# Kernel tuning notes

Measured on AMD Instinct MI355X. Metric: run time of the kernel, lower is better.

Reference implementation:

```python
import jax, jax.numpy as jnp
import numpy as np
from jax import lax

N, P = 64, 7
C1, H1 = 256, 56
C2, H2 = 512, 28
C3, H3 = 1024, 14
HID1, HID2, HID3 = 256, 768, 1792
MLP1, MLP2, OUT = 3584, 1792, 512


def setup_inputs() -> dict:
    key = jax.random.key(0)
    ks = jax.random.split(key, 32)
    x1 = jax.random.normal(ks[0], (N, C1, H1, H1), jnp.float32)
    x2 = jax.random.normal(ks[1], (N, C2, H2, H2), jnp.float32)
    x3 = jax.random.normal(ks[2], (N, C3, H3, H3), jnp.float32)
    a = jax.random.randint(ks[3], (N, P, 2), 0, 56)
    b = jax.random.randint(ks[4], (N, P, 2), 0, 56)
    lo, hi = jnp.minimum(a, b), jnp.maximum(a, b)
    patchs = jnp.stack([lo[..., 0], hi[..., 0], lo[..., 1], hi[..., 1]], axis=-1)
    drop = jax.random.bernoulli(ks[5], 0.1, (N, P))
    patchs = jnp.where(drop[..., None], 0, patchs).astype(jnp.int32)

    def lin(k, o, i):
        return jax.random.normal(k, (o, i), jnp.float32) * 0.02

    def vec(k, o):
        return jax.random.normal(k, (o,), jnp.float32) * 0.02

    inp = {
        'x1': x1, 'x2': x2, 'x3': x3, 'patchs': patchs,
        # LSTM weights, torch gate order (i,f,g,o); bias = b_ih + b_hh combined
        'l1_wih': lin(ks[6], 4 * HID1, 256),  'l1_whh': lin(ks[7], 4 * HID1, HID1),  'l1_b': vec(ks[8], 4 * HID1),
        'l2_wih': lin(ks[9], 4 * HID2, 768),  'l2_whh': lin(ks[10], 4 * HID2, HID2), 'l2_b': vec(ks[11], 4 * HID2),
        'l3_wih': lin(ks[12], 4 * HID3, 1792),'l3_whh': lin(ks[13], 4 * HID3, HID3), 'l3_b': vec(ks[14], 4 * HID3),
        'aw1': lin(ks[15], MLP1, P * HID3), 'ab1': vec(ks[16], MLP1),
        'aw2': lin(ks[17], MLP2, MLP1),     'ab2': vec(ks[18], MLP2),
        'aw3': lin(ks[19], P, MLP2),        'ab3': vec(ks[20], P),
        'fw':  lin(ks[21], OUT, HID3),      'fb':  vec(ks[22], OUT),
    }
    return inp


def _crop_avg(x, patchs, num, den):
    """Batched data-dependent crop + avg-pool via 2D integral image.
    x: [N,C,H,W]; patchs: [N,P,4] ints (y0,y1,x0,x1) at 56-scale. Returns [N,P,C]."""
    y0 = (patchs[..., 0] * num) // den
    y1 = (patchs[..., 1] * num) // den
    x0 = (patchs[..., 2] * num) // den
    x1 = (patchs[..., 3] * num) // den
    S = jnp.cumsum(jnp.cumsum(x, axis=2), axis=3)
    S = jnp.pad(S, ((0, 0), (0, 0), (1, 0), (1, 0)))  # [N,C,H+1,W+1]
    bidx = jnp.arange(x.shape[0])[:, None]

    def g(Y, X):
        return S[bidx, :, Y, X]  # advanced idx split by ':' -> [N,P,C]

    tot = g(y1 + 1, x1 + 1) - g(y0, x1 + 1) - g(y1 + 1, x0) + g(y0, x0)
    area = ((y1 - y0 + 1) * (x1 - x0 + 1)).astype(x.dtype)[..., None]
    avg = tot / area
    zero = jnp.all(patchs == 0, axis=-1)  # all-zero box -> zero feature
    return jnp.where(zero[..., None], jnp.zeros((), x.dtype), avg)


def _lstm(x, wih, whh, b):
    """Single-layer batch-first LSTM, torch gate order i,f,g,o. x: [N,T,D] -> [N,T,H]."""
    Nb, T, _ = x.shape
    H = whh.shape[1]
    xg = jnp.einsum('ntd,gd->ntg', x, wih) + b  # precompute input gates

    def step(carry, xt):
        h, c = carry
        gates = xt + h @ whh.T
        i, f, g, o = jnp.split(gates, 4, axis=-1)
        c = jax.nn.sigmoid(f) * c + jax.nn.sigmoid(i) * jnp.tanh(g)
        h = jax.nn.sigmoid(o) * jnp.tanh(c)
        return (h, c), h

    h0 = jnp.zeros((Nb, H), x.dtype)
    _, hs = lax.scan(step, (h0, h0), jnp.swapaxes(xg, 0, 1))
    return jnp.swapaxes(hs, 0, 1)


def reference(x1, x2, x3, patchs,
              l1_wih, l1_whh, l1_b, l2_wih, l2_whh, l2_b, l3_wih, l3_whh, l3_b,
              aw1, ab1, aw2, ab2, aw3, ab3, fw, fb):
    local1 = _crop_avg(x1, patchs, 55, 55)                     # [N,7,256]
    rnn1 = _lstm(local1, l1_wih, l1_whh, l1_b)                 # [N,7,256]
    local2 = jnp.concatenate([_crop_avg(x2, patchs, 27, 55), rnn1], axis=2)   # [N,7,768]
    rnn2 = _lstm(local2, l2_wih, l2_whh, l2_b)                 # [N,7,768]
    local3 = jnp.concatenate([_crop_avg(x3, patchs, 13, 55), rnn2], axis=2)   # [N,7,1792]
    rnn3 = _lstm(local3, l3_wih, l3_whh, l3_b)                 # [N,7,1792]
    # attention pooling (dropout = identity in eval)
    flat = rnn3.reshape(rnn3.shape[0], -1)                     # [N,7*1792]
    h = jax.nn.relu(flat @ aw1.T + ab1)
    h = jax.nn.relu(h @ aw2.T + ab2)
    attn = jax.nn.relu(h @ aw3.T + ab3)                        # [N,7]
    alpha = jax.nn.softmax(attn, axis=1)
    feat = jnp.sum(rnn3 * alpha[:, :, None], axis=1)           # [N,1792]
    return feat @ fw.T + fb                                    # [N,512]
```

## Files before the change

### kernel.cpp

```cpp
#include <hip/hip_runtime.h>
#include <hip/hip_bf16.h>
#include <math.h>

#define NB 64
#define PP 7

typedef __attribute__((ext_vector_type(8))) short short8;
typedef __attribute__((ext_vector_type(4))) float f32x4;

static __device__ inline unsigned bf16r(float f) {
    unsigned u = __builtin_bit_cast(unsigned, f);
    u += 0x7fffu + ((u >> 16) & 1u);
    return u >> 16;
}
static __device__ inline unsigned pack2(float a, float b) {
    return bf16r(a) | (bf16r(b) << 16);
}

template<int H, int VEC, int GRP>
__device__ inline void crop_dev(
    int bx, int n, const float* __restrict__ x, const int* __restrict__ patchs,
    float* __restrict__ out, int C, int num, int den, int ldo, int col0)
{
    constexpr int USED = H / VEC;
    constexpr int PPWAVE = 64 / GRP;
    int tid = threadIdx.x, lane = tid & 63, wv = tid >> 6;
    int sub = lane / GRP, xl = lane & (GRP - 1);
    bool act = xl < USED;
    int c = bx * (4 * PPWAVE) + wv * PPWAVE + sub;

    int y0s[PP], yds[PP], x0s[PP], x1s[PP], zer[PP];
    float rarea[PP];
    #pragma unroll
    for (int p = 0; p < PP; ++p) {
        int p0 = patchs[(n * PP + p) * 4 + 0];
        int p1 = patchs[(n * PP + p) * 4 + 1];
        int p2 = patchs[(n * PP + p) * 4 + 2];
        int p3 = patchs[(n * PP + p) * 4 + 3];
        int y0 = p0 * num / den, y1 = p1 * num / den;
        int xx0 = p2 * num / den, xx1 = p3 * num / den;
        y0s[p] = y0; yds[p] = y1 - y0;
        x0s[p] = xx0; x1s[p] = xx1;
        rarea[p] = 1.f / (float)((y1 - y0 + 1) * (xx1 - xx0 + 1));
        zer[p] = (p0 | p1 | p2 | p3) == 0;
    }

    const float* pl = x + ((size_t)n * C + c) * (H * H) + (act ? xl * VEC : 0);

    float acc[PP][VEC];
    #pragma unroll
    for (int p = 0; p < PP; ++p)
        #pragma unroll
        for (int e = 0; e < VEC; ++e) acc[p][e] = 0.f;

    #pragma unroll 4
    for (int y = 0; y < H; ++y) {
        float v[VEC];
        if constexpr (VEC == 4) {
            float4 t = *reinterpret_cast<const float4*>(pl + y * H);
            v[0] = t.x; v[1] = t.y; v[2] = t.z; v[3] = t.w;
        } else {
            float2 t = *reinterpret_cast<const float2*>(pl + y * H);
            v[0] = t.x; v[1] = t.y;
        }
        #pragma unroll
        for (int p = 0; p < PP; ++p) {
            float m = ((unsigned)(y - y0s[p]) <= (unsigned)yds[p]) ? 1.f : 0.f;
            #pragma unroll
            for (int e = 0; e < VEC; ++e)
                acc[p][e] = fmaf(m, v[e], acc[p][e]);
        }
    }

    #pragma unroll
    for (int p = 0; p < PP; ++p) {
        float d = 0.f;
        #pragma unroll
        for (int e = 0; e < VEC; ++e) {
            int col = xl * VEC + e;
            if (col >= x0s[p] && col <= x1s[p]) d += acc[p][e];
        }
        #pragma unroll
        for (int off = GRP / 2; off >= 1; off >>= 1)
            d += __shfl_xor(d, off, 64);
        if (act && xl == 0)
            out[(size_t)(n * PP + p) * ldo + col0 + c] = zer[p] ? 0.f : d * rarea[p];
    }
}

__device__ inline void cvt_dev(
    int b, const float* __restrict__ in, uint4* __restrict__ out, int n8)
{
    int idx = b * 256 + threadIdx.x;
    if (idx >= n8) return;
    const float4* p = reinterpret_cast<const float4*>(in) + 2 * (size_t)idx;
    float4 a = p[0], bb = p[1];
    uint4 v;
    v.x = pack2(a.x, a.y); v.y = pack2(a.z, a.w);
    v.z = pack2(bb.x, bb.y); v.w = pack2(bb.z, bb.w);
    out[idx] = v;
}

__global__ __launch_bounds__(256) void prep_kernel(
    const float* __restrict__ x1, const float* __restrict__ x2,
    const float* __restrict__ x3, const int* __restrict__ patchs,
    float* __restrict__ local1, float* __restrict__ local2,
    float* __restrict__ local3,
    const float* __restrict__ l1_whh, uint4* __restrict__ whh1b,
    const float* __restrict__ l2_whh, uint4* __restrict__ whh2b,
    const float* __restrict__ l3_whh, uint4* __restrict__ whh3b)
{
    int b = blockIdx.x;
    if (b < 1024) {
        crop_dev<56, 4, 16>(b & 15, b >> 4, x1, patchs, local1, 256, 55, 55, 256, 0);
    } else if (b < 2048) {
        int bb = b - 1024;
        crop_dev<28, 4, 8>(bb & 15, bb >> 4, x2, patchs, local2, 512, 27, 55, 768, 0);
    } else if (b < 4096) {
        int bb = b - 2048;
        crop_dev<14, 2, 8>(bb & 31, bb >> 5, x3, patchs, local3, 1024, 13, 55, 1792, 0);
    } else if (b < 4224) {
        cvt_dev(b - 4096, l1_whh, whh1b, 32768);
    } else if (b < 5376) {
        cvt_dev(b - 4224, l2_whh, whh2b, 294912);
    } else {
        cvt_dev(b - 5376, l3_whh, whh3b, 1605632);
    }
}

template<int BN, bool WBF>
__global__ __launch_bounds__(256) void gemm_kernel(
    const float* __restrict__ X, int ldx,
    const void* __restrict__ Wp, int K,
    const float* __restrict__ bias,
    float* __restrict__ out, int ldo,
    int kchunk, int partial)
{
    constexpr int NF = BN / 64;
    __shared__ short Xs[64][72];
    __shared__ short Ws[BN][72];
    int tid = threadIdx.x;
    int lane = tid & 63, wv = tid >> 6;
    int m0 = blockIdx.y * 64;
    int o0 = blockIdx.x * BN;
    int z = blockIdx.z;
    int kbeg = z * kchunk, kend = kbeg + kchunk;

    f32x4 acc[4][NF];
    #pragma unroll
    for (int i = 0; i < 4; ++i)
        #pragma unroll
        for (int j = 0; j < NF; ++j)
            acc[i][j] = (f32x4){0.f, 0.f, 0.f, 0.f};

    for (int kb = kbeg; kb < kend; kb += 64) {
        #pragma unroll
        for (int i = 0; i < 2; ++i) {
            int cch = tid + 256 * i;
            int r = cch >> 3, col = (cch & 7) * 8;
            const float* src = X + (size_t)(m0 + r) * ldx + kb + col;
            float4 a = *reinterpret_cast<const float4*>(src);
            float4 b = *reinterpret_cast<const float4*>(src + 4);
            uint4 v;
            v.x = pack2(a.x, a.y); v.y = pack2(a.z, a.w);
            v.z = pack2(b.x, b.y); v.w = pack2(b.z, b.w);
            *reinterpret_cast<uint4*>(&Xs[r][col]) = v;
        }
        #pragma unroll
        for (int i = 0; i < 2 * NF; ++i) {
            int cch = tid + 256 * i;
            int r = cch >> 3, col = (cch & 7) * 8;
            if constexpr (WBF) {
                const short* srcw = (const short*)Wp + (size_t)(o0 + r) * K + kb + col;
                *reinterpret_cast<uint4*>(&Ws[r][col]) =
                    *reinterpret_cast<const uint4*>(srcw);
            } else {
                const float* srcw = (const float*)Wp + (size_t)(o0 + r) * K + kb + col;
                float4 c = *reinterpret_cast<const float4*>(srcw);
                float4 d = *reinterpret_cast<const float4*>(srcw + 4);
                uint4 w;
                w.x = pack2(c.x, c.y); w.y = pack2(c.z, c.w);
                w.z = pack2(d.x, d.y); w.w = pack2(d.z, d.w);
                *reinterpret_cast<uint4*>(&Ws[r][col]) = w;
            }
        }
        __syncthreads();
        #pragma unroll
        for (int kk = 0; kk < 64; kk += 32) {
            int ro = lane & 15, kof = kk + (lane >> 4) * 8;
            short8 b[NF];
            #pragma unroll
            for (int j = 0; j < NF; ++j)
                b[j] = *reinterpret_cast<const short8*>(
                    &Ws[wv * (BN / 4) + 16 * j + ro][kof]);
            #pragma unroll
            for (int i = 0; i < 4; ++i) {
                short8 a = *reinterpret_cast<const short8*>(&Xs[16 * i + ro][kof]);
                #pragma unroll
                for (int j = 0; j < NF; ++j)
                    acc[i][j] = __builtin_amdgcn_mfma_f32_16x16x32_bf16(
                        a, b[j], acc[i][j], 0, 0, 0);
            }
        }
        __syncthreads();
    }

    float* dst = out;
    if (partial) dst += (size_t)z * (gridDim.y * 64) * ldo;
    int mr = (lane >> 4) * 4;
    #pragma unroll
    for (int j = 0; j < NF; ++j) {
        int o = o0 + wv * (BN / 4) + 16 * j + (lane & 15);
        float bv = (!partial && bias) ? bias[o] : 0.f;
        #pragma unroll
        for (int i = 0; i < 4; ++i) {
            #pragma unroll
            for (int r = 0; r < 4; ++r) {
                int m = m0 + 16 * i + mr + r;
                dst[(size_t)m * ldo + o] = acc[i][j][r] + bv;
            }
        }
    }
}

__global__ __launch_bounds__(256) void reduce_kernel(
    const float* __restrict__ partial, int S, int M, int O,
    const float* __restrict__ bias, int relu, float* __restrict__ out)
{
    int idx = blockIdx.x * 256 + threadIdx.x;
    int tot = M * O;
    if (idx >= tot) return;
    float v = bias[idx % O];
    for (int s = 0; s < S; ++s) v += partial[(size_t)s * tot + idx];
    if (relu) v = fmaxf(v, 0.f);
    out[idx] = v;
}

__global__ __launch_bounds__(256) void lstm_cell_kernel(
    const float* __restrict__ partial, int S,
    const float* __restrict__ xgt, int ldxg,
    float* __restrict__ h, float* __restrict__ c,
    float* __restrict__ dest, int Hd, int ldd, int first)
{
    int idx = blockIdx.x * 256 + threadIdx.x;
    int q = Hd >> 2;
    if (idx >= NB * q) return;
    int n = idx / q, j4 = (idx - n * q) * 4;
    int H4 = 4 * Hd;

    f32x4 g[4];
    #pragma unroll
    for (int gi = 0; gi < 4; ++gi)
        g[gi] = *reinterpret_cast<const f32x4*>(xgt + (size_t)n * ldxg + gi * Hd + j4);
    if (!first) {
        for (int s = 0; s < S; ++s) {
            const float* pr = partial + ((size_t)s * NB + n) * H4;
            #pragma unroll
            for (int gi = 0; gi < 4; ++gi)
                g[gi] += *reinterpret_cast<const f32x4*>(pr + gi * Hd + j4);
        }
    }
    f32x4 cp = (f32x4){0.f, 0.f, 0.f, 0.f};
    if (!first) cp = *reinterpret_cast<const f32x4*>(c + (size_t)n * Hd + j4);

    f32x4 cn, hn;
    #pragma unroll
    for (int k = 0; k < 4; ++k) {
        float si = 1.f / (1.f + expf(-g[0][k]));
        float sf = 1.f / (1.f + expf(-g[1][k]));
        float so = 1.f / (1.f + expf(-g[3][k]));
        float cc = sf * cp[k] + si * tanhf(g[2][k]);
        cn[k] = cc;
        hn[k] = so * tanhf(cc);
    }
    *reinterpret_cast<f32x4*>(c + (size_t)n * Hd + j4) = cn;
    *reinterpret_cast<f32x4*>(h + (size_t)n * Hd + j4) = hn;
    *reinterpret_cast<f32x4*>(dest + (size_t)n * ldd + j4) = hn;
}

__global__ __launch_bounds__(256) void attn_fused_kernel(
    const float* __restrict__ h2, const float* __restrict__ aw3,
    const float* __restrict__ ab3, const float* __restrict__ rnn3,
    float* __restrict__ feat)
{
    int n = blockIdx.x;
    int tid = threadIdx.x, lane = tid & 63, wv = tid >> 6;
    __shared__ float logit[PP];
    __shared__ float alpha[PP];
    for (int p = wv; p < PP; p += 4) {
        float s = 0.f;
        for (int k = lane; k < 1792; k += 64)
            s += h2[n * 1792 + k] * aw3[p * 1792 + k];
        #pragma unroll
        for (int off = 32; off; off >>= 1) s += __shfl_down(s, off, 64);
        if (lane == 0) logit[p] = fmaxf(s + ab3[p], 0.f);
    }
    __syncthreads();
    if (tid == 0) {
        float a[PP], mx = -1e30f;
        for (int p = 0; p < PP; ++p) { a[p] = logit[p]; mx = fmaxf(mx, a[p]); }
        float s = 0.f;
        for (int p = 0; p < PP; ++p) { a[p] = expf(a[p] - mx); s += a[p]; }
        for (int p = 0; p < PP; ++p) alpha[p] = a[p] / s;
    }
    __syncthreads();
    for (int j = tid; j < 1792; j += 256) {
        float s = 0.f;
        #pragma unroll
        for (int p = 0; p < PP; ++p)
            s += rnn3[((size_t)n * PP + p) * 1792 + j] * alpha[p];
        feat[(size_t)n * 1792 + j] = s;
    }
}


extern "C" void kernel_launch(void* const* d_in, const int* in_sizes, int n_in,
                              void* d_out, int out_size, void* d_ws, size_t ws_size,
                              hipStream_t stream) {
    const float* x1 = (const float*)d_in[0];
    const float* x2 = (const float*)d_in[1];
    const float* x3 = (const float*)d_in[2];
    const int* patchs = (const int*)d_in[3];
    const float* l1_wih = (const float*)d_in[4];
    const float* l1_whh = (const float*)d_in[5];
    const float* l1_b   = (const float*)d_in[6];
    const float* l2_wih = (const float*)d_in[7];
    const float* l2_whh = (const float*)d_in[8];
    const float* l2_b   = (const float*)d_in[9];
    const float* l3_wih = (const float*)d_in[10];
    const float* l3_whh = (const float*)d_in[11];
    const float* l3_b   = (const float*)d_in[12];
    const float* aw1 = (const float*)d_in[13];
    const float* ab1 = (const float*)d_in[14];
    const float* aw2 = (const float*)d_in[15];
    const float* ab2 = (const float*)d_in[16];
    const float* aw3 = (const float*)d_in[17];
    const float* ab3 = (const float*)d_in[18];
    const float* fw  = (const float*)d_in[19];
    const float* fb  = (const float*)d_in[20];
    float* out = (float*)d_out;

    float* ws = (float*)d_ws;
    float* local1 = ws;
    float* local2 = local1 + 114688;
    float* local3 = local2 + 344064;
    float* rnn3   = local3;
    float* xg     = local3 + 802816;
    float* partial= xg + 3211264;
    float* hbuf   = partial + 3211264;
    float* cbuf   = hbuf + 114688;
    float* h1     = cbuf + 114688;
    float* h2     = h1 + 229376;
    float* feat   = h2 + 114688;
    float* wb     = feat + 114688;
    short* whh1b  = (short*)wb;
    short* whh2b  = (short*)(wb + 131072);
    short* whh3b  = (short*)(wb + 131072 + 1179648);

    prep_kernel<<<11648, 256, 0, stream>>>(
        x1, x2, x3, patchs, local1, local2, local3,
        l1_whh, (uint4*)whh1b, l2_whh, (uint4*)whh2b, l3_whh, (uint4*)whh3b);

    {
        int H = 256, H4 = 1024;
        gemm_kernel<64, false><<<dim3(16, 7, 1), 256, 0, stream>>>(
            local1, 256, l1_wih, 256, l1_b, xg, H4, 256, 0);
        for (int t = 0; t < PP; ++t) {
            if (t > 0)
                gemm_kernel<64, true><<<dim3(16, 1, 4), 256, 0, stream>>>(
                    hbuf, H, whh1b, H, nullptr, partial, H4, 64, 1);
            lstm_cell_kernel<<<(NB * H / 4 + 255) / 256, 256, 0, stream>>>(
                partial, 4, xg + (size_t)t * H4, PP * H4,
                hbuf, cbuf, local2 + (size_t)t * 768 + 512, H, PP * 768, t == 0);
        }
    }
    {
        int H = 768, H4 = 3072;
        gemm_kernel<64, false><<<dim3(48, 7, 1), 256, 0, stream>>>(
            local2, 768, l2_wih, 768, l2_b, xg, H4, 768, 0);
        for (int t = 0; t < PP; ++t) {
            if (t > 0)
                gemm_kernel<64, true><<<dim3(48, 1, 6), 256, 0, stream>>>(
                    hbuf, H, whh2b, H, nullptr, partial, H4, 128, 1);
            lstm_cell_kernel<<<(NB * H / 4 + 255) / 256, 256, 0, stream>>>(
                partial, 6, xg + (size_t)t * H4, PP * H4,
                hbuf, cbuf, local3 + (size_t)t * 1792 + 1024, H, PP * 1792, t == 0);
        }
    }
    {
        int H = 1792, H4 = 7168;
        gemm_kernel<128, false><<<dim3(56, 7, 1), 256, 0, stream>>>(
            local3, 1792, l3_wih, 1792, l3_b, xg, H4, 1792, 0);
        for (int t = 0; t < PP; ++t) {
            if (t > 0)
                gemm_kernel<128, true><<<dim3(56, 1, 7), 256, 0, stream>>>(
                    hbuf, H, whh3b, H, nullptr, partial, H4, 256, 1);
            lstm_cell_kernel<<<(NB * H / 4 + 255) / 256, 256, 0, stream>>>(
                partial, 7, xg + (size_t)t * H4, PP * H4,
                hbuf, cbuf, rnn3 + (size_t)t * 1792, H, PP * 1792, t == 0);
        }
    }

    gemm_kernel<64, false><<<dim3(56, 1, 14), 256, 0, stream>>>(
        rnn3, 12544, aw1, 12544, nullptr, partial, 3584, 896, 1);
    reduce_kernel<<<(64 * 3584 + 255) / 256, 256, 0, stream>>>(
        partial, 14, 64, 3584, ab1, 1, h1);
    gemm_kernel<64, false><<<dim3(28, 1, 7), 256, 0, stream>>>(
        h1, 3584, aw2, 3584, nullptr, partial, 1792, 512, 1);
    reduce_kernel<<<(64 * 1792 + 255) / 256, 256, 0, stream>>>(
        partial, 7, 64, 1792, ab2, 1, h2);
    attn_fused_kernel<<<NB, 256, 0, stream>>>(h2, aw3, ab3, rnn3, feat);
    gemm_kernel<64, false><<<dim3(8, 1, 7), 256, 0, stream>>>(
        feat, 1792, fw, 1792, nullptr, partial, 512, 256, 1);
    reduce_kernel<<<(64 * 512 + 255) / 256, 256, 0, stream>>>(
        partial, 7, 64, 512, fb, 0, out);
}
```

Before: 605.9 us.

## Fuse layer-1 LSTM recurrence into one persistent per-batch kernel

Replaces the per-timestep loop of recurrent GEMM launches plus cell-update launches for the first LSTM layer with a single kernel that has one block per batch row. The block keeps h in LDS and c in registers, and computes the hidden-state matvec with bf16 weights on plain FMAs. This removes about 13 kernel launches and the round-trips of partial sums through global memory. In exchange each block rereads the whole 256x1024 bf16 weight matrix from cache every step without matrix cores, and only 64 blocks are used.

```diff
diff --git a/kernel.cpp b/kernel.cpp
--- a/kernel.cpp
+++ b/kernel.cpp
@@ -15,6 +15,9 @@
 }
 static __device__ inline unsigned pack2(float a, float b) {
     return bf16r(a) | (bf16r(b) << 16);
+}
+static __device__ inline float bf2f(short s) {
+    return __builtin_bit_cast(float, ((unsigned)(unsigned short)s) << 16);
 }
 
 template<int H, int VEC, int GRP>
@@ -220,6 +223,58 @@
                 dst[(size_t)m * ldo + o] = acc[i][j][r] + bv;
             }
         }
+    }
+}
+
+__global__ __launch_bounds__(256) void lstm_l1_kernel(
+    const short* __restrict__ whhb,
+    const float* __restrict__ xg,
+    float* __restrict__ local2)
+{
+    __shared__ float h_lds[256];
+    __shared__ float gbuf[1024];
+    int n = blockIdx.x, tid = threadIdx.x;
+    float creg = 0.f;
+
+    for (int t = 0; t < PP; ++t) {
+        const float* xrow = xg + (size_t)(n * PP + t) * 1024;
+        float gi_, gf_, gg_, go_;
+        if (t == 0) {
+            gi_ = xrow[tid]; gf_ = xrow[256 + tid];
+            gg_ = xrow[512 + tid]; go_ = xrow[768 + tid];
+        } else {
+            float acc[4] = {0.f, 0.f, 0.f, 0.f};
+            for (int k8 = 0; k8 < 256; k8 += 8) {
+                float hv[8];
+                #pragma unroll
+                for (int e = 0; e < 8; ++e) hv[e] = h_lds[k8 + e];
+                #pragma unroll
+                for (int r = 0; r < 4; ++r) {
+                    int o = tid * 4 + r;
+                    short8 w = *reinterpret_cast<const short8*>(
+                        whhb + (size_t)o * 256 + k8);
+                    #pragma unroll
+                    for (int e = 0; e < 8; ++e)
+                        acc[r] = fmaf(bf2f(w[e]), hv[e], acc[r]);
+                }
+            }
+            #pragma unroll
+            for (int r = 0; r < 4; ++r) gbuf[tid * 4 + r] = acc[r];
+            __syncthreads();
+            gi_ = xrow[tid] + gbuf[tid];
+            gf_ = xrow[256 + tid] + gbuf[256 + tid];
+            gg_ = xrow[512 + tid] + gbuf[512 + tid];
+            go_ = xrow[768 + tid] + gbuf[768 + tid];
+        }
+        float si = 1.f / (1.f + expf(-gi_));
+        float sf = 1.f / (1.f + expf(-gf_));
+        float so = 1.f / (1.f + expf(-go_));
+        creg = sf * creg + si * tanhf(gg_);
+        float hn = so * tanhf(creg);
+        if (t > 0) __syncthreads();
+        h_lds[tid] = hn;
+        local2[(size_t)(n * PP + t) * 768 + 512 + tid] = hn;
+        __syncthreads();
     }
 }
 
@@ -362,17 +417,10 @@
         l1_whh, (uint4*)whh1b, l2_whh, (uint4*)whh2b, l3_whh, (uint4*)whh3b);
 
     {
-        int H = 256, H4 = 1024;
+        int H4 = 1024;
         gemm_kernel<64, false><<<dim3(16, 7, 1), 256, 0, stream>>>(
             local1, 256, l1_wih, 256, l1_b, xg, H4, 256, 0);
-        for (int t = 0; t < PP; ++t) {
-            if (t > 0)
-                gemm_kernel<64, true><<<dim3(16, 1, 4), 256, 0, stream>>>(
-                    hbuf, H, whh1b, H, nullptr, partial, H4, 64, 1);
-            lstm_cell_kernel<<<(NB * H / 4 + 255) / 256, 256, 0, stream>>>(
-                partial, 4, xg + (size_t)t * H4, PP * H4,
-                hbuf, cbuf, local2 + (size_t)t * 768 + 512, H, PP * 768, t == 0);
-        }
+        lstm_l1_kernel<<<64, 256, 0, stream>>>(whh1b, xg, local2);
     }
     {
         int H = 768, H4 = 3072;
```

Result: slower. 655.2 us (+8.1%).
